# Kernel tuning notes

Measured on AMD Instinct MI355X. Metric: run time of the kernel, lower is better.

## Reference

```python
import jax, jax.numpy as jnp
import numpy as np

OT_REG = 0.1
OT_ITERS = 10
LN_EPS = 1e-5


def layernorm(x, g, b):
    m = jnp.mean(x, axis=-1, keepdims=True)
    v = jnp.mean((x - m) ** 2, axis=-1, keepdims=True)
    return (x - m) * jax.lax.rsqrt(v + LN_EPS) * g + b


def sinkhorn(C, epsilon, iters):
    # standard Sinkhorn: kernel exp(C/eps), alternate row/col normalization
    Q = jnp.exp(C / epsilon)  # [Na,B,La,Lb]
    def body(_, Q):
        Q = Q / jnp.sum(Q, axis=-1, keepdims=True)
        Q = Q / jnp.sum(Q, axis=-2, keepdims=True)
        return Q
    return jax.lax.fori_loop(0, iters, body, Q)


def setup_inputs() -> dict:
    key = jax.random.key(0)
    ks = jax.random.split(key, 16)
    Na, La, B, Lb, Din, H = 32, 32, 64, 32, 768, 768
    s = 0.02
    return {
        "entity_cls": jax.random.normal(ks[0], (Na, Din), jnp.float32),
        "entity_tokens": jax.random.normal(ks[1], (Na, La, Din), jnp.float32),
        "mention_cls": jax.random.normal(ks[2], (B, Din), jnp.float32),
        "mention_tokens": jax.random.normal(ks[3], (B, Lb, Din), jnp.float32),
        "Wq": jax.random.normal(ks[4], (Din, H), jnp.float32) * s,
        "bq": jnp.zeros((H,), jnp.float32),
        "Wk": jax.random.normal(ks[5], (Din, H), jnp.float32) * s,
        "bk": jnp.zeros((H,), jnp.float32),
        "Wv": jax.random.normal(ks[6], (Din, H), jnp.float32) * s,
        "bv": jnp.zeros((H,), jnp.float32),
        "ln1_g": jnp.ones((H,), jnp.float32),
        "ln1_b": jnp.zeros((H,), jnp.float32),
        "Wcls": jax.random.normal(ks[7], (Din, H), jnp.float32) * s,
        "bcls": jnp.zeros((H,), jnp.float32),
        "Wsp": jax.random.normal(ks[8], (H, 1), jnp.float32) * s,
        "bsp": jnp.zeros((1,), jnp.float32),
        "ln2_g": jnp.ones((H,), jnp.float32),
        "ln2_b": jnp.zeros((H,), jnp.float32),
    }


def reference(entity_cls, entity_tokens, mention_cls, mention_tokens,
              Wq, bq, Wk, bk, Wv, bv, ln1_g, ln1_b,
              Wcls, bcls, Wsp, bsp, ln2_g, ln2_b):
    # projections
    q = entity_tokens @ Wq + bq      # [Na,La,H]
    k = mention_tokens @ Wk + bk     # [B,Lb,H]
    v = mention_tokens @ Wv + bv     # [B,Lb,H]

    # cross-batch cosine similarity: [Na,B,La,Lb]
    qn = q / jnp.maximum(jnp.linalg.norm(q, axis=-1, keepdims=True), 1e-8)
    kn = k / jnp.maximum(jnp.linalg.norm(k, axis=-1, keepdims=True), 1e-8)
    C = jnp.einsum('aid,bjd->abij', qn, kn)

    # Sinkhorn on detached cost (torch uses C.detach())
    T = sinkhorn(jax.lax.stop_gradient(C), OT_REG, OT_ITERS)
    # F.normalize(dim=-1): L2 normalize last dim
    T = T / jnp.maximum(jnp.linalg.norm(T, axis=-1, keepdims=True), 1e-12)

    # attention + residual + layernorm: [Na,B,La,H]
    attended = jnp.einsum('abij,bjd->abid', T, v) + q[:, None, :, :]
    attended = layernorm(attended, ln1_g, ln1_b)

    # softpool over token dim (-2)
    w = jax.nn.softmax(attended @ Wsp + bsp, axis=-2)   # [Na,B,La,1]
    pooled = jnp.sum(attended * w, axis=-2)             # [Na,B,H]
    context = layernorm(pooled, ln2_g, ln2_b)

    # matching scores
    ecls = entity_cls @ Wcls + bcls                     # [Na,H]
    g2l = jnp.sum(ecls[:, None, :] * context, axis=-1)  # [Na,B]
    g2l = g2l.T                                         # [B,Na]
    g2g = mention_cls @ entity_cls.T                    # [B,Na]
    return (g2l + g2g) * 0.5
```

## Files before the change

kernel.cpp:

```cpp
#include <hip/hip_runtime.h>
#include <math.h>


typedef __attribute__((ext_vector_type(8))) short bfrag8;
typedef __attribute__((ext_vector_type(4))) float f32x4;

__device__ __forceinline__ unsigned short f2bf(float x) {
  union { float f; unsigned u; } v; v.f = x;
  unsigned r = v.u + 0x7fffu + ((v.u >> 16) & 1u);
  return (unsigned short)(r >> 16);
}

template <int CTRL>
__device__ __forceinline__ float dpp_add(float x) {
  union { float f; int i; } a, b;
  a.f = x;
  b.i = __builtin_amdgcn_update_dpp(0, a.i, CTRL, 0xf, 0xf, true);
  return x + b.f;
}
__device__ __forceinline__ float sum16(float x) {
  x = dpp_add<0xB1>(x);
  x = dpp_add<0x4E>(x);
  x = dpp_add<0x124>(x);
  x = dpp_add<0x128>(x);
  return x;
}

__global__ __launch_bounds__(256) void prep_kernel(
    const float* __restrict__ a0, const float* __restrict__ a1, const float* __restrict__ a2,
    unsigned short* __restrict__ o0, unsigned short* __restrict__ o1, unsigned short* __restrict__ o2,
    float* __restrict__ nrm,
    const float* __restrict__ W0, const float* __restrict__ W1,
    const float* __restrict__ W2, const float* __restrict__ W3,
    unsigned short* __restrict__ T0, unsigned short* __restrict__ T1,
    unsigned short* __restrict__ T2, unsigned short* __restrict__ T3) {
  __shared__ float t[32][33];
  int bx = blockIdx.x;
  if (bx < 2331) {
    if (bx < 2328) {
      const float* in; unsigned short* out; int i, n4;
      if (bx < 768)       { in = a0; out = o0; i = bx * 256 + threadIdx.x;          n4 = 196608; }
      else if (bx < 2304) { in = a1; out = o1; i = (bx - 768) * 256 + threadIdx.x;  n4 = 393216; }
      else                { in = a2; out = o2; i = (bx - 2304) * 256 + threadIdx.x; n4 = 6144; }
      if (i >= n4) return;
      float4 f = ((const float4*)in)[i];
      ushort4 o;
      o.x = f2bf(f.x); o.y = f2bf(f.y); o.z = f2bf(f.z); o.w = f2bf(f.w);
      ((ushort4*)out)[i] = o;
    } else {
      int i = (bx - 2328) * 256 + threadIdx.x;
      if (i < 768) ((float4*)nrm)[i] = make_float4(0.f, 0.f, 0.f, 0.f);
    }
    return;
  }
  int idx = bx - 2331;
  int z = idx / 576, r2 = idx % 576;
  int tby = r2 / 24, tbx = r2 % 24;
  const float* W = (z == 0) ? W0 : (z == 1) ? W1 : (z == 2) ? W2 : W3;
  unsigned short* O = (z == 0) ? T0 : (z == 1) ? T1 : (z == 2) ? T2 : T3;
  const int gx = tbx * 32, gy = tby * 32;
  const int tx = threadIdx.x & 31, ty = threadIdx.x >> 5;
#pragma unroll
  for (int u = 0; u < 4; ++u) {
    int row = ty + u * 8;
    t[row][tx] = W[(size_t)(gy + row) * 768 + gx + tx];
  }
  __syncthreads();
#pragma unroll
  for (int u = 0; u < 4; ++u) {
    int row = ty + u * 8;
    O[(size_t)(gx + row) * 768 + gy + tx] = f2bf(t[tx][row]);
  }
}

__global__ __launch_bounds__(512, 2) void proj_gemm_kernel(
    const unsigned short* __restrict__ Ae, const unsigned short* __restrict__ Am,
    const unsigned short* __restrict__ Acls,
    const unsigned short* __restrict__ WqT, const unsigned short* __restrict__ WkT,
    const unsigned short* __restrict__ WvT, const unsigned short* __restrict__ WclsT,
    const float* __restrict__ bq, const float* __restrict__ bk,
    const float* __restrict__ bv, const float* __restrict__ bcls,
    unsigned short* __restrict__ qb, unsigned short* __restrict__ qT,
    unsigned short* __restrict__ kb, unsigned short* __restrict__ vT,
    float* __restrict__ ecls, float* __restrict__ iq_sq, float* __restrict__ ik_sq) {
  const int z = blockIdx.z;
  const int M = (z == 0) ? 1024 : (z == 3) ? 32 : 2048;
  const int bm = blockIdx.y * 128;
  if (bm >= M) return;
  const unsigned short* A = (z == 3) ? Acls : (z == 0) ? Ae : Am;
  const unsigned short* B = (z == 0) ? WqT : (z == 1) ? WkT : (z == 2) ? WvT : WclsT;
  const float* bias = (z == 0) ? bq : (z == 1) ? bk : (z == 2) ? bv : bcls;

  __shared__ unsigned short As[128 * 64];
  __shared__ unsigned short Bs[128 * 64];
  const int t = threadIdx.x;
  const int bn = blockIdx.x * 128;
  const int l = t & 63, w = t >> 6;
  const int wm = w & 3, wn = w >> 2;
  const int cg = l & 15, rq = l >> 4;

  f32x4 acc[2][4];
#pragma unroll
  for (int mi = 0; mi < 2; ++mi)
#pragma unroll
    for (int nj = 0; nj < 4; ++nj) { f32x4 zz = {0.f, 0.f, 0.f, 0.f}; acc[mi][nj] = zz; }

  for (int k0 = 0; k0 < 768; k0 += 64) {
    __syncthreads();
#pragma unroll
    for (int u = 0; u < 2; ++u) {
      int c = t + u * 512;
      int row = c >> 3, kc = c & 7;
      int gm = bm + row; gm = gm < M ? gm : M - 1;
      int4 av = *(const int4*)(A + (size_t)gm * 768 + k0 + kc * 8);
      *(int4*)(As + row * 64 + ((kc ^ (row & 7)) * 8)) = av;
      int4 bv4 = *(const int4*)(B + (size_t)(bn + row) * 768 + k0 + kc * 8);
      *(int4*)(Bs + row * 64 + ((kc ^ (row & 7)) * 8)) = bv4;
    }
    __syncthreads();
#pragma unroll
    for (int kk = 0; kk < 2; ++kk) {
      bfrag8 af[2], bf[4];
      const int kc = kk * 4 + rq;
#pragma unroll
      for (int mi = 0; mi < 2; ++mi) {
        int arow = wm * 32 + mi * 16 + cg;
        af[mi] = *(const bfrag8*)(As + arow * 64 + ((kc ^ (arow & 7)) * 8));
      }
#pragma unroll
      for (int nj = 0; nj < 4; ++nj) {
        int brow = wn * 64 + nj * 16 + cg;
        bf[nj] = *(const bfrag8*)(Bs + brow * 64 + ((kc ^ (brow & 7)) * 8));
      }
#pragma unroll
      for (int mi = 0; mi < 2; ++mi)
#pragma unroll
        for (int nj = 0; nj < 4; ++nj)
          acc[mi][nj] = __builtin_amdgcn_mfma_f32_16x16x32_bf16(af[mi], bf[nj], acc[mi][nj], 0, 0, 0);
    }
  }

  float p[2][4] = {};
#pragma unroll
  for (int mi = 0; mi < 2; ++mi) {
#pragma unroll
    for (int nj = 0; nj < 4; ++nj) {
      int gn = bn + wn * 64 + nj * 16 + cg;
      float bs = bias[gn];
#pragma unroll
      for (int r = 0; r < 4; ++r) {
        int gm = bm + wm * 32 + mi * 16 + rq * 4 + r;
        if (gm >= M) continue;
        float val = acc[mi][nj][r] + bs;
        if (z < 2) p[mi][r] += val * val;
        unsigned short bfv = f2bf(val);
        if (z == 0) {
          qb[(size_t)gm * 768 + gn] = bfv;
          int at = gm >> 5, j = gm & 31;
          qT[((size_t)at * 768 + gn) * 32 + j] = bfv;
        } else if (z == 1) kb[(size_t)gm * 768 + gn] = bfv;
        else if (z == 2) {
          int bb = gm >> 5, j = gm & 31;
          vT[((size_t)bb * 768 + gn) * 32 + j] = bfv;
        } else ecls[(size_t)gm * 768 + gn] = val;
      }
    }
  }
  if (z < 2) {
    float* nrm = (z == 0) ? iq_sq : ik_sq;
#pragma unroll
    for (int mi = 0; mi < 2; ++mi)
#pragma unroll
      for (int r = 0; r < 4; ++r) {
        float s = sum16(p[mi][r]);
        if (cg == 0) {
          int gm = bm + wm * 32 + mi * 16 + rq * 4 + r;
          atomicAdd(&nrm[gm], s);
        }
      }
  }
}

__global__ __launch_bounds__(512, 2) void cos_attn_kernel(
    const unsigned short* __restrict__ qb, const unsigned short* __restrict__ kb,
    const float* __restrict__ iq_sq, const float* __restrict__ ik_sq,
    const unsigned short* __restrict__ qT,
    const unsigned short* __restrict__ vT,
    const float* __restrict__ ln1_g, const float* __restrict__ ln1_b,
    const float* __restrict__ Wsp, const float* __restrict__ bsp,
    const float* __restrict__ ln2_g, const float* __restrict__ ln2_b,
    const float* __restrict__ ecls,
    const float* __restrict__ entity_cls, const float* __restrict__ mention_cls,
    float* __restrict__ out) {
  __shared__ unsigned short vLds[2 * 768 * 32];
  __shared__ __align__(16) unsigned short scratch[12288];
  __shared__ float gabLds[4 * 768];
  __shared__ float gwLds[768];
  __shared__ float ldsIq[128], ldsIk[64];
  __shared__ float red[80];

  unsigned short* As = scratch;
  unsigned short* Bs = scratch + 8192;
  unsigned short* Tlds = scratch;

  const int t = threadIdx.x;
  const int l = t & 63, w = t >> 6;
  const int bm = blockIdx.y * 128, bn = blockIdx.x * 64;
  const int wm = w & 3, wn = w >> 2;
  const int cg = l & 15, rq = l >> 4;

  {
    float sgw = 0.f, sbw = 0.f, sga[4] = {}, sba[4] = {};
    for (int h = t; h < 768; h += 512) {
      float g1 = ln1_g[h], b1 = ln1_b[h], wsp = Wsp[h];
      float g2 = ln2_g[h], b2 = ln2_b[h];
      float gw = g1 * wsp;
      gwLds[h] = gw;
      sgw += gw; sbw += b1 * wsp;
#pragma unroll
      for (int aa = 0; aa < 4; ++aa) {
        float ec = ecls[(size_t)((blockIdx.y << 2) + aa) * 768 + h];
        float gab = g2 * ec;
        gabLds[aa * 768 + h] = gab;
        sga[aa] += gab; sba[aa] += b2 * ec;
      }
    }
    sgw = sum16(sgw); sbw = sum16(sbw);
#pragma unroll
    for (int aa = 0; aa < 4; ++aa) { sga[aa] = sum16(sga[aa]); sba[aa] = sum16(sba[aa]); }
#pragma unroll
    for (int m = 16; m < 64; m <<= 1) {
      sgw += __shfl_xor(sgw, m); sbw += __shfl_xor(sbw, m);
#pragma unroll
      for (int aa = 0; aa < 4; ++aa) { sga[aa] += __shfl_xor(sga[aa], m); sba[aa] += __shfl_xor(sba[aa], m); }
    }
    if (l == 0) {
      red[w * 10 + 0] = sgw; red[w * 10 + 1] = sbw;
#pragma unroll
      for (int aa = 0; aa < 4; ++aa) { red[w * 10 + 2 + aa] = sga[aa]; red[w * 10 + 6 + aa] = sba[aa]; }
    }
  }
  if (t < 128) ldsIq[t] = iq_sq[bm + t];
  else if (t < 192) ldsIk[t - 128] = ik_sq[bn + t - 128];

  const int4* vsrc = (const int4*)(vT + (size_t)(blockIdx.x * 2) * 768 * 32);
  int4* vdst = (int4*)vLds;

  f32x4 acc[2][2];
#pragma unroll
  for (int mi = 0; mi < 2; ++mi)
#pragma unroll
    for (int nj = 0; nj < 2; ++nj) { f32x4 zz = {0.f, 0.f, 0.f, 0.f}; acc[mi][nj] = zz; }

  for (int k0 = 0, s = 0; k0 < 768; k0 += 64, ++s) {
    __syncthreads();
#pragma unroll
    for (int u = 0; u < 2; ++u) {
      int c = t + u * 512;
      int row = c >> 3, kc = c & 7;
      int4 av = *(const int4*)(qb + (size_t)(bm + row) * 768 + k0 + kc * 8);
      *(int4*)(As + row * 64 + ((kc ^ (row & 7)) * 8)) = av;
    }
    {
      int row = t >> 3, kc = t & 7;
      int4 bv4 = *(const int4*)(kb + (size_t)(bn + row) * 768 + k0 + kc * 8);
      *(int4*)(Bs + row * 64 + ((kc ^ (row & 7)) * 8)) = bv4;
    }
    vdst[t + s * 512] = vsrc[t + s * 512];
    __syncthreads();
#pragma unroll
    for (int kk = 0; kk < 2; ++kk) {
      bfrag8 af[2], bf[2];
      const int kc = kk * 4 + rq;
#pragma unroll
      for (int mi = 0; mi < 2; ++mi) {
        int arow = wm * 32 + mi * 16 + cg;
        af[mi] = *(const bfrag8*)(As + arow * 64 + ((kc ^ (arow & 7)) * 8));
      }
#pragma unroll
      for (int nj = 0; nj < 2; ++nj) {
        int brow = wn * 32 + nj * 16 + cg;
        bf[nj] = *(const bfrag8*)(Bs + brow * 64 + ((kc ^ (brow & 7)) * 8));
      }
#pragma unroll
      for (int mi = 0; mi < 2; ++mi)
#pragma unroll
        for (int nj = 0; nj < 2; ++nj)
          acc[mi][nj] = __builtin_amdgcn_mfma_f32_16x16x32_bf16(af[mi], bf[nj], acc[mi][nj], 0, 0, 0);
    }
  }

  float irow[2][4], icol[2];
#pragma unroll
  for (int mi = 0; mi < 2; ++mi)
#pragma unroll
    for (int r = 0; r < 4; ++r) {
      float sv = ldsIq[wm * 32 + mi * 16 + rq * 4 + r];
      irow[mi][r] = 1.0f / fmaxf(sqrtf(sv), 1e-8f);
    }
#pragma unroll
  for (int nj = 0; nj < 2; ++nj) {
    float sv = ldsIk[wn * 32 + nj * 16 + cg];
    icol[nj] = 1.0f / fmaxf(sqrtf(sv), 1e-8f);
  }
#pragma unroll
  for (int mi = 0; mi < 2; ++mi)
#pragma unroll
    for (int nj = 0; nj < 2; ++nj)
#pragma unroll
      for (int r = 0; r < 4; ++r)
        acc[mi][nj][r] = __expf(acc[mi][nj][r] * irow[mi][r] * icol[nj] * 10.0f);

  for (int it = 0; it < 10; ++it) {
#pragma unroll
    for (int mi = 0; mi < 2; ++mi)
#pragma unroll
      for (int r = 0; r < 4; ++r) {
        float rs = sum16(acc[mi][0][r] + acc[mi][1][r]);
        float rinv = __builtin_amdgcn_rcpf(rs);
        acc[mi][0][r] *= rinv; acc[mi][1][r] *= rinv;
      }
#pragma unroll
    for (int nj = 0; nj < 2; ++nj) {
      float cs = acc[0][nj][0] + acc[0][nj][1] + acc[0][nj][2] + acc[0][nj][3]
               + acc[1][nj][0] + acc[1][nj][1] + acc[1][nj][2] + acc[1][nj][3];
      cs += __shfl_xor(cs, 16); cs += __shfl_xor(cs, 32);
      float cinv = __builtin_amdgcn_rcpf(cs);
#pragma unroll
      for (int mi = 0; mi < 2; ++mi)
#pragma unroll
        for (int r = 0; r < 4; ++r) acc[mi][nj][r] *= cinv;
    }
  }

#pragma unroll
  for (int mi = 0; mi < 2; ++mi)
#pragma unroll
    for (int r = 0; r < 4; ++r) {
      float ss = sum16(acc[mi][0][r] * acc[mi][0][r] + acc[mi][1][r] * acc[mi][1][r]);
      float tinv = 1.0f / fmaxf(sqrtf(ss), 1e-12f);
      acc[mi][0][r] *= tinv; acc[mi][1][r] *= tinv;
    }

  __syncthreads();
  {
    unsigned short* base = Tlds + ((wn * 4 + wm) << 10);
#pragma unroll
    for (int mi = 0; mi < 2; ++mi)
#pragma unroll
      for (int nj = 0; nj < 2; ++nj)
#pragma unroll
        for (int r = 0; r < 4; ++r)
          base[(mi * 16 + rq * 4 + r) * 32 + nj * 16 + cg] = f2bf(acc[mi][nj][r]);
  }
  __syncthreads();

  const int bl = w & 1, ah = w >> 1;
  const int b_g = (blockIdx.x << 1) + bl;
  const int a_g = (blockIdx.y << 2) + ah;
  const unsigned short* vbase = vLds + bl * 24576;

  float sgw_f = 0.f, sbw_f = 0.f, sga_f = 0.f, sba_f = 0.f;
#pragma unroll
  for (int wv = 0; wv < 8; ++wv) {
    sgw_f += red[wv * 10 + 0]; sbw_f += red[wv * 10 + 1];
    sga_f += red[wv * 10 + 2 + ah]; sba_f += red[wv * 10 + 6 + ah];
  }
  sbw_f += bsp[0];

  const unsigned short* qTa = qT + (size_t)a_g * 24576;
  const unsigned short* Tp = Tlds + ((bl * 4 + ah) << 10);
  bfrag8 af[2], afI[2];
#pragma unroll
  for (int mi = 0; mi < 2; ++mi) {
    af[mi] = *(const bfrag8*)(Tp + (mi * 16 + cg) * 32 + rq * 8);
    int row = mi * 16 + cg;
    bfrag8 fI;
#pragma unroll
    for (int u = 0; u < 8; ++u) fI[u] = (row == rq * 8 + u) ? (short)0x3F80 : (short)0;
    afI[mi] = fI;
  }

  float s1[2][4] = {}, s2[2][4] = {}, a1[2][4] = {};
#pragma unroll 4
  for (int nj = 0; nj < 48; ++nj) {
    int h = nj * 16 + cg;
    bfrag8 vf = *(const bfrag8*)(vbase + h * 32 + rq * 8);
    bfrag8 qf = *(const bfrag8*)(qTa + (size_t)h * 32 + rq * 8);
    float gw = gwLds[h];
#pragma unroll
    for (int mi = 0; mi < 2; ++mi) {
      f32x4 zz = {0.f, 0.f, 0.f, 0.f};
      f32x4 p = __builtin_amdgcn_mfma_f32_16x16x32_bf16(af[mi], vf, zz, 0, 0, 0);
      f32x4 x4 = __builtin_amdgcn_mfma_f32_16x16x32_bf16(afI[mi], qf, p, 0, 0, 0);
#pragma unroll
      for (int r = 0; r < 4; ++r) {
        float x = x4[r];
        s1[mi][r] += x; s2[mi][r] += x * x; a1[mi][r] += x * gw;
      }
    }
  }
#pragma unroll
  for (int mi = 0; mi < 2; ++mi)
#pragma unroll
    for (int r = 0; r < 4; ++r) {
      s1[mi][r] = sum16(s1[mi][r]);
      s2[mi][r] = sum16(s2[mi][r]);
      a1[mi][r] = sum16(a1[mi][r]);
    }

  float uu[2][4], c0;
  {
    float mean[2][4], rstd[2][4], logit[2][4];
#pragma unroll
    for (int mi = 0; mi < 2; ++mi)
#pragma unroll
      for (int r = 0; r < 4; ++r) {
        float m1 = s1[mi][r] * (1.0f / 768.0f);
        float var = s2[mi][r] * (1.0f / 768.0f) - m1 * m1;
        float rs = rsqrtf(var + 1e-5f);
        mean[mi][r] = m1; rstd[mi][r] = rs;
        logit[mi][r] = rs * (a1[mi][r] - m1 * sgw_f) + sbw_f;
      }
    float mx = logit[0][0];
#pragma unroll
    for (int mi = 0; mi < 2; ++mi)
#pragma unroll
      for (int r = 0; r < 4; ++r) mx = fmaxf(mx, logit[mi][r]);
    mx = fmaxf(mx, __shfl_xor(mx, 16)); mx = fmaxf(mx, __shfl_xor(mx, 32));
    float se = 0.f, ee[2][4];
#pragma unroll
    for (int mi = 0; mi < 2; ++mi)
#pragma unroll
      for (int r = 0; r < 4; ++r) { ee[mi][r] = __expf(logit[mi][r] - mx); se += ee[mi][r]; }
    se += __shfl_xor(se, 16); se += __shfl_xor(se, 32);
    const float sinv = __builtin_amdgcn_rcpf(se);
    float c0a = 0.f;
#pragma unroll
    for (int mi = 0; mi < 2; ++mi)
#pragma unroll
      for (int r = 0; r < 4; ++r) {
        uu[mi][r] = ee[mi][r] * sinv * rstd[mi][r];
        c0a += uu[mi][r] * mean[mi][r];
      }
    c0a += __shfl_xor(c0a, 16); c0a += __shfl_xor(c0a, 32);
    c0 = c0a;
  }

  float ps = 0.f, pq = 0.f, spc = 0.f;
#pragma unroll 4
  for (int nj = 0; nj < 48; ++nj) {
    int h = nj * 16 + cg;
    bfrag8 vf = *(const bfrag8*)(vbase + h * 32 + rq * 8);
    bfrag8 qf = *(const bfrag8*)(qTa + (size_t)h * 32 + rq * 8);
    float pp = 0.f;
#pragma unroll
    for (int mi = 0; mi < 2; ++mi) {
      f32x4 zz = {0.f, 0.f, 0.f, 0.f};
      f32x4 p = __builtin_amdgcn_mfma_f32_16x16x32_bf16(af[mi], vf, zz, 0, 0, 0);
      f32x4 x4 = __builtin_amdgcn_mfma_f32_16x16x32_bf16(afI[mi], qf, p, 0, 0, 0);
#pragma unroll
      for (int r = 0; r < 4; ++r) pp += uu[mi][r] * x4[r];
    }
    pp += __shfl_xor(pp, 16); pp += __shfl_xor(pp, 32);
    float pooled = ln1_g[h] * (pp - c0) + ln1_b[h];
    ps += pooled; pq += pooled * pooled;
    spc += pooled * gabLds[ah * 768 + h];
  }
  ps = sum16(ps); pq = sum16(pq); spc = sum16(spc);
  const float m2 = ps * (1.0f / 768.0f);
  const float var2 = pq * (1.0f / 768.0f) - m2 * m2;
  const float rs2 = rsqrtf(var2 + 1e-5f);
  const float* ea = entity_cls + (size_t)a_g * 768;
  const float* mb = mention_cls + (size_t)b_g * 768;
  float sg = 0.f;
#pragma unroll
  for (int u = 0; u < 12; ++u) sg += mb[l * 12 + u] * ea[l * 12 + u];
  sg = sum16(sg);
  sg += __shfl_xor(sg, 16); sg += __shfl_xor(sg, 32);
  float tot = rs2 * (spc - m2 * sga_f) + sba_f + sg;
  if (l == 0) out[b_g * 32 + a_g] = 0.5f * tot;
}

extern "C" void kernel_launch(void* const* d_in, const int* in_sizes, int n_in,
                              void* d_out, int out_size, void* d_ws, size_t ws_size,
                              hipStream_t stream) {
  const float* entity_cls     = (const float*)d_in[0];
  const float* entity_tokens  = (const float*)d_in[1];
  const float* mention_cls    = (const float*)d_in[2];
  const float* mention_tokens = (const float*)d_in[3];
  const float* Wq = (const float*)d_in[4];   const float* bq = (const float*)d_in[5];
  const float* Wk = (const float*)d_in[6];   const float* bk = (const float*)d_in[7];
  const float* Wv = (const float*)d_in[8];   const float* bv = (const float*)d_in[9];
  const float* ln1_g = (const float*)d_in[10]; const float* ln1_b = (const float*)d_in[11];
  const float* Wcls = (const float*)d_in[12];  const float* bcls = (const float*)d_in[13];
  const float* Wsp = (const float*)d_in[14];   const float* bsp = (const float*)d_in[15];
  const float* ln2_g = (const float*)d_in[16]; const float* ln2_b = (const float*)d_in[17];
  float* out = (float*)d_out;

  float* ws     = (float*)d_ws;
  float* ecls   = ws;
  float* iq_sq  = ecls + 24576;
  float* ik_sq  = iq_sq + 1024;
  unsigned short* qb = (unsigned short*)(ws + 55168);
  unsigned short* qT = qb + 786432;
  unsigned short* kb = qT + 786432;
  unsigned short* vT = kb + 1572864;
  char* R = (char*)(vT + 1572864);
  unsigned short* Ae    = (unsigned short*)R;
  unsigned short* Am    = Ae + 786432;
  unsigned short* Acls  = Am + 1572864;
  unsigned short* WqT   = Acls + 24576;
  unsigned short* WkT   = WqT + 589824;
  unsigned short* WvT   = WkT + 589824;
  unsigned short* WclsT = WvT + 589824;

  prep_kernel<<<dim3(4635), dim3(256), 0, stream>>>(
      entity_tokens, mention_tokens, entity_cls, Ae, Am, Acls, iq_sq,
      Wq, Wk, Wv, Wcls, WqT, WkT, WvT, WclsT);
  proj_gemm_kernel<<<dim3(6, 16, 4), dim3(512), 0, stream>>>(
      Ae, Am, Acls, WqT, WkT, WvT, WclsT, bq, bk, bv, bcls,
      qb, qT, kb, vT, ecls, iq_sq, ik_sq);
  cos_attn_kernel<<<dim3(32, 8), dim3(512), 0, stream>>>(
      qb, kb, iq_sq, ik_sq, qT, vT,
      ln1_g, ln1_b, Wsp, bsp, ln2_g, ln2_b,
      ecls, entity_cls, mention_cls, out);
}
```

Baseline: 166.1 us.

## Double cos_attn block to 1024 threads, splitting each warp's work across wave pairs

```diff
diff --git a/kernel.cpp b/kernel.cpp
--- a/kernel.cpp
+++ b/kernel.cpp
@@ -181,7 +181,7 @@
   }
 }
 
-__global__ __launch_bounds__(512, 2) void cos_attn_kernel(
+__global__ __launch_bounds__(1024, 4) void cos_attn_kernel(
     const unsigned short* __restrict__ qb, const unsigned short* __restrict__ kb,
     const float* __restrict__ iq_sq, const float* __restrict__ ik_sq,
     const unsigned short* __restrict__ qT,
@@ -197,7 +197,8 @@
   __shared__ float gabLds[4 * 768];
   __shared__ float gwLds[768];
   __shared__ float ldsIq[128], ldsIk[64];
-  __shared__ float red[80];
+  __shared__ float red[160];
+  __shared__ float xch[1584];
 
   unsigned short* As = scratch;
   unsigned short* Bs = scratch + 8192;
@@ -205,13 +206,14 @@
 
   const int t = threadIdx.x;
   const int l = t & 63, w = t >> 6;
+  const int p = w >> 1, q = w & 1;
   const int bm = blockIdx.y * 128, bn = blockIdx.x * 64;
-  const int wm = w & 3, wn = w >> 2;
+  const int wm = p & 3, wn = p >> 2;
   const int cg = l & 15, rq = l >> 4;
 
   {
     float sgw = 0.f, sbw = 0.f, sga[4] = {}, sba[4] = {};
-    for (int h = t; h < 768; h += 512) {
+    for (int h = t; h < 768; h += 1024) {
       float g1 = ln1_g[h], b1 = ln1_b[h], wsp = Wsp[h];
       float g2 = ln2_g[h], b2 = ln2_b[h];
       float gw = g1 * wsp;
@@ -246,130 +248,118 @@
   const int4* vsrc = (const int4*)(vT + (size_t)(blockIdx.x * 2) * 768 * 32);
   int4* vdst = (int4*)vLds;
 
-  f32x4 acc[2][2];
-#pragma unroll
-  for (int mi = 0; mi < 2; ++mi)
-#pragma unroll
-    for (int nj = 0; nj < 2; ++nj) { f32x4 zz = {0.f, 0.f, 0.f, 0.f}; acc[mi][nj] = zz; }
+  f32x4 acc[2];
+#pragma unroll
+  for (int nj = 0; nj < 2; ++nj) { f32x4 zz = {0.f, 0.f, 0.f, 0.f}; acc[nj] = zz; }
 
   for (int k0 = 0, s = 0; k0 < 768; k0 += 64, ++s) {
     __syncthreads();
-#pragma unroll
-    for (int u = 0; u < 2; ++u) {
-      int c = t + u * 512;
-      int row = c >> 3, kc = c & 7;
+    {
+      int row = t >> 3, kc = t & 7;
       int4 av = *(const int4*)(qb + (size_t)(bm + row) * 768 + k0 + kc * 8);
       *(int4*)(As + row * 64 + ((kc ^ (row & 7)) * 8)) = av;
     }
-    {
+    if (t < 512) {
       int row = t >> 3, kc = t & 7;
       int4 bv4 = *(const int4*)(kb + (size_t)(bn + row) * 768 + k0 + kc * 8);
       *(int4*)(Bs + row * 64 + ((kc ^ (row & 7)) * 8)) = bv4;
-    }
-    vdst[t + s * 512] = vsrc[t + s * 512];
+    } else {
+      int tt = t - 512;
+      vdst[tt + s * 512] = vsrc[tt + s * 512];
+    }
     __syncthreads();
 #pragma unroll
     for (int kk = 0; kk < 2; ++kk) {
-      bfrag8 af[2], bf[2];
       const int kc = kk * 4 + rq;
-#pragma unroll
-      for (int mi = 0; mi < 2; ++mi) {
-        int arow = wm * 32 + mi * 16 + cg;
-        af[mi] = *(const bfrag8*)(As + arow * 64 + ((kc ^ (arow & 7)) * 8));
-      }
+      const int arow = wm * 32 + q * 16 + cg;
+      bfrag8 af = *(const bfrag8*)(As + arow * 64 + ((kc ^ (arow & 7)) * 8));
+      bfrag8 bf[2];
 #pragma unroll
       for (int nj = 0; nj < 2; ++nj) {
         int brow = wn * 32 + nj * 16 + cg;
         bf[nj] = *(const bfrag8*)(Bs + brow * 64 + ((kc ^ (brow & 7)) * 8));
       }
 #pragma unroll
-      for (int mi = 0; mi < 2; ++mi)
-#pragma unroll
-        for (int nj = 0; nj < 2; ++nj)
-          acc[mi][nj] = __builtin_amdgcn_mfma_f32_16x16x32_bf16(af[mi], bf[nj], acc[mi][nj], 0, 0, 0);
-    }
-  }
-
-  float irow[2][4], icol[2];
-#pragma unroll
-  for (int mi = 0; mi < 2; ++mi)
-#pragma unroll
-    for (int r = 0; r < 4; ++r) {
-      float sv = ldsIq[wm * 32 + mi * 16 + rq * 4 + r];
-      irow[mi][r] = 1.0f / fmaxf(sqrtf(sv), 1e-8f);
-    }
+      for (int nj = 0; nj < 2; ++nj)
+        acc[nj] = __builtin_amdgcn_mfma_f32_16x16x32_bf16(af, bf[nj], acc[nj], 0, 0, 0);
+    }
+  }
+
+  float irow[4], icol[2];
+#pragma unroll
+  for (int r = 0; r < 4; ++r) {
+    float sv = ldsIq[wm * 32 + q * 16 + rq * 4 + r];
+    irow[r] = 1.0f / fmaxf(sqrtf(sv), 1e-8f);
+  }
 #pragma unroll
   for (int nj = 0; nj < 2; ++nj) {
     float sv = ldsIk[wn * 32 + nj * 16 + cg];
     icol[nj] = 1.0f / fmaxf(sqrtf(sv), 1e-8f);
   }
 #pragma unroll
-  for (int mi = 0; mi < 2; ++mi)
-#pragma unroll
-    for (int nj = 0; nj < 2; ++nj)
-#pragma unroll
-      for (int r = 0; r < 4; ++r)
-        acc[mi][nj][r] = __expf(acc[mi][nj][r] * irow[mi][r] * icol[nj] * 10.0f);
+  for (int nj = 0; nj < 2; ++nj)
+#pragma unroll
+    for (int r = 0; r < 4; ++r)
+      acc[nj][r] = __expf(acc[nj][r] * irow[r] * icol[nj] * 10.0f);
 
   for (int it = 0; it < 10; ++it) {
 #pragma unroll
-    for (int mi = 0; mi < 2; ++mi)
-#pragma unroll
-      for (int r = 0; r < 4; ++r) {
-        float rs = sum16(acc[mi][0][r] + acc[mi][1][r]);
-        float rinv = __builtin_amdgcn_rcpf(rs);
-        acc[mi][0][r] *= rinv; acc[mi][1][r] *= rinv;
-      }
+    for (int r = 0; r < 4; ++r) {
+      float rs = sum16(acc[0][r] + acc[1][r]);
+      float rinv = __builtin_amdgcn_rcpf(rs);
+      acc[0][r] *= rinv; acc[1][r] *= rinv;
+    }
+    float colp[2];
 #pragma unroll
     for (int nj = 0; nj < 2; ++nj) {
-      float cs = acc[0][nj][0] + acc[0][nj][1] + acc[0][nj][2] + acc[0][nj][3]
-               + acc[1][nj][0] + acc[1][nj][1] + acc[1][nj][2] + acc[1][nj][3];
-      cs += __shfl_xor(cs, 16); cs += __shfl_xor(cs, 32);
+      float cl = acc[nj][0] + acc[nj][1] + acc[nj][2] + acc[nj][3];
+      cl += __shfl_xor(cl, 16); cl += __shfl_xor(cl, 32);
+      colp[nj] = cl;
+      if (rq == 0) xch[(it & 1) * 512 + w * 32 + nj * 16 + cg] = cl;
+    }
+    __syncthreads();
+#pragma unroll
+    for (int nj = 0; nj < 2; ++nj) {
+      float cs = colp[nj] + xch[(it & 1) * 512 + (w ^ 1) * 32 + nj * 16 + cg];
       float cinv = __builtin_amdgcn_rcpf(cs);
 #pragma unroll
-      for (int mi = 0; mi < 2; ++mi)
-#pragma unroll
-        for (int r = 0; r < 4; ++r) acc[mi][nj][r] *= cinv;
-    }
-  }
-
-#pragma unroll
-  for (int mi = 0; mi < 2; ++mi)
-#pragma unroll
-    for (int r = 0; r < 4; ++r) {
-      float ss = sum16(acc[mi][0][r] * acc[mi][0][r] + acc[mi][1][r] * acc[mi][1][r]);
-      float tinv = 1.0f / fmaxf(sqrtf(ss), 1e-12f);
-      acc[mi][0][r] *= tinv; acc[mi][1][r] *= tinv;
-    }
+      for (int r = 0; r < 4; ++r) acc[nj][r] *= cinv;
+    }
+  }
+
+#pragma unroll
+  for (int r = 0; r < 4; ++r) {
+    float ss = sum16(acc[0][r] * acc[0][r] + acc[1][r] * acc[1][r]);
+    float tinv = 1.0f / fmaxf(sqrtf(ss), 1e-12f);
+    acc[0][r] *= tinv; acc[1][r] *= tinv;
+  }
 
   __syncthreads();
   {
-    unsigned short* base = Tlds + ((wn * 4 + wm) << 10);
-#pragma unroll
-    for (int mi = 0; mi < 2; ++mi)
-#pragma unroll
-      for (int nj = 0; nj < 2; ++nj)
-#pragma unroll
-        for (int r = 0; r < 4; ++r)
-          base[(mi * 16 + rq * 4 + r) * 32 + nj * 16 + cg] = f2bf(acc[mi][nj][r]);
+    unsigned short* base = Tlds + (p << 10);
+#pragma unroll
+    for (int nj = 0; nj < 2; ++nj)
+#pragma unroll
+      for (int r = 0; r < 4; ++r)
+        base[(q * 16 + rq * 4 + r) * 32 + nj * 16 + cg] = f2bf(acc[nj][r]);
   }
   __syncthreads();
 
-  const int bl = w & 1, ah = w >> 1;
+  const int bl = p >> 2, ah = p & 3;
   const int b_g = (blockIdx.x << 1) + bl;
   const int a_g = (blockIdx.y << 2) + ah;
   const unsigned short* vbase = vLds + bl * 24576;
 
   float sgw_f = 0.f, sbw_f = 0.f, sga_f = 0.f, sba_f = 0.f;
 #pragma unroll
-  for (int wv = 0; wv < 8; ++wv) {
+  for (int wv = 0; wv < 16; ++wv) {
     sgw_f += red[wv * 10 + 0]; sbw_f += red[wv * 10 + 1];
     sga_f += red[wv * 10 + 2 + ah]; sba_f += red[wv * 10 + 6 + ah];
   }
   sbw_f += bsp[0];
 
   const unsigned short* qTa = qT + (size_t)a_g * 24576;
-  const unsigned short* Tp = Tlds + ((bl * 4 + ah) << 10);
+  const unsigned short* Tp = Tlds + (p << 10);
   bfrag8 af[2], afI[2];
 #pragma unroll
   for (int mi = 0; mi < 2; ++mi) {
@@ -383,7 +373,8 @@
 
   float s1[2][4] = {}, s2[2][4] = {}, a1[2][4] = {};
 #pragma unroll 4
-  for (int nj = 0; nj < 48; ++nj) {
+  for (int j = 0; j < 24; ++j) {
+    int nj = q * 24 + j;
     int h = nj * 16 + cg;
     bfrag8 vf = *(const bfrag8*)(vbase + h * 32 + rq * 8);
     bfrag8 qf = *(const bfrag8*)(qTa + (size_t)h * 32 + rq * 8);
@@ -391,8 +382,8 @@
 #pragma unroll
     for (int mi = 0; mi < 2; ++mi) {
       f32x4 zz = {0.f, 0.f, 0.f, 0.f};
-      f32x4 p = __builtin_amdgcn_mfma_f32_16x16x32_bf16(af[mi], vf, zz, 0, 0, 0);
-      f32x4 x4 = __builtin_amdgcn_mfma_f32_16x16x32_bf16(afI[mi], qf, p, 0, 0, 0);
+      f32x4 pr = __builtin_amdgcn_mfma_f32_16x16x32_bf16(af[mi], vf, zz, 0, 0, 0);
+      f32x4 x4 = __builtin_amdgcn_mfma_f32_16x16x32_bf16(afI[mi], qf, pr, 0, 0, 0);
 #pragma unroll
       for (int r = 0; r < 4; ++r) {
         float x = x4[r];
@@ -408,6 +399,30 @@
       s2[mi][r] = sum16(s2[mi][r]);
       a1[mi][r] = sum16(a1[mi][r]);
     }
+  if (cg == 0) {
+#pragma unroll
+    for (int mi = 0; mi < 2; ++mi)
+#pragma unroll
+      for (int r = 0; r < 4; ++r) {
+        int row = mi * 16 + rq * 4 + r;
+        xch[(w * 3 + 0) * 32 + row] = s1[mi][r];
+        xch[(w * 3 + 1) * 32 + row] = s2[mi][r];
+        xch[(w * 3 + 2) * 32 + row] = a1[mi][r];
+      }
+  }
+  __syncthreads();
+  {
+    const int pw = w ^ 1;
+#pragma unroll
+    for (int mi = 0; mi < 2; ++mi)
+#pragma unroll
+      for (int r = 0; r < 4; ++r) {
+        int row = mi * 16 + rq * 4 + r;
+        s1[mi][r] += xch[(pw * 3 + 0) * 32 + row];
+        s2[mi][r] += xch[(pw * 3 + 1) * 32 + row];
+        a1[mi][r] += xch[(pw * 3 + 2) * 32 + row];
+      }
+  }
 
   float uu[2][4], c0;
   {
@@ -449,7 +464,8 @@
 
   float ps = 0.f, pq = 0.f, spc = 0.f;
 #pragma unroll 4
-  for (int nj = 0; nj < 48; ++nj) {
+  for (int j = 0; j < 24; ++j) {
+    int nj = q * 24 + j;
     int h = nj * 16 + cg;
     bfrag8 vf = *(const bfrag8*)(vbase + h * 32 + rq * 8);
     bfrag8 qf = *(const bfrag8*)(qTa + (size_t)h * 32 + rq * 8);
@@ -457,8 +473,8 @@
 #pragma unroll
     for (int mi = 0; mi < 2; ++mi) {
       f32x4 zz = {0.f, 0.f, 0.f, 0.f};
-      f32x4 p = __builtin_amdgcn_mfma_f32_16x16x32_bf16(af[mi], vf, zz, 0, 0, 0);
-      f32x4 x4 = __builtin_amdgcn_mfma_f32_16x16x32_bf16(afI[mi], qf, p, 0, 0, 0);
+      f32x4 pr = __builtin_amdgcn_mfma_f32_16x16x32_bf16(af[mi], vf, zz, 0, 0, 0);
+      f32x4 x4 = __builtin_amdgcn_mfma_f32_16x16x32_bf16(afI[mi], qf, pr, 0, 0, 0);
 #pragma unroll
       for (int r = 0; r < 4; ++r) pp += uu[mi][r] * x4[r];
     }
@@ -468,6 +484,18 @@
     spc += pooled * gabLds[ah * 768 + h];
   }
   ps = sum16(ps); pq = sum16(pq); spc = sum16(spc);
+  if (l == 0) {
+    xch[1536 + w * 3 + 0] = ps;
+    xch[1536 + w * 3 + 1] = pq;
+    xch[1536 + w * 3 + 2] = spc;
+  }
+  __syncthreads();
+  {
+    const int pw = w ^ 1;
+    ps += xch[1536 + pw * 3 + 0];
+    pq += xch[1536 + pw * 3 + 1];
+    spc += xch[1536 + pw * 3 + 2];
+  }
   const float m2 = ps * (1.0f / 768.0f);
   const float var2 = pq * (1.0f / 768.0f) - m2 * m2;
   const float rs2 = rsqrtf(var2 + 1e-5f);
@@ -479,7 +507,7 @@
   sg = sum16(sg);
   sg += __shfl_xor(sg, 16); sg += __shfl_xor(sg, 32);
   float tot = rs2 * (spc - m2 * sga_f) + sba_f + sg;
-  if (l == 0) out[b_g * 32 + a_g] = 0.5f * tot;
+  if (l == 0 && q == 0) out[b_g * 32 + a_g] = 0.5f * tot;
 }
 
 extern "C" void kernel_launch(void* const* d_in, const int* in_sizes, int n_in,
@@ -521,7 +549,7 @@
   proj_gemm_kernel<<<dim3(6, 16, 4), dim3(512), 0, stream>>>(
       Ae, Am, Acls, WqT, WkT, WvT, WclsT, bq, bk, bv, bcls,
       qb, qT, kb, vT, ecls, iq_sq, ik_sq);
-  cos_attn_kernel<<<dim3(32, 8), dim3(512), 0, stream>>>(
+  cos_attn_kernel<<<dim3(32, 8), dim3(1024), 0, stream>>>(
       qb, kb, iq_sq, ik_sq, qT, vT,
       ln1_g, ln1_b, Wsp, bsp, ln2_g, ln2_b,
       ecls, entity_cls, mention_cls, out);
```

New measurement: 185.8 us. 1.12x slower.
